# Performance work log

Measured on AMD Instinct MI355X. Metric: run time of the kernel, lower is better.

## Reference

```python
import jax, jax.numpy as jnp
import numpy as np

# config dims (see shape_source)
NO = 8        # Max_Object
NT = 32       # Max_Time
C = 512       # feat_dims
VD = 1024     # visual_dim
RD = 300      # self.nfeat (relation word-vector dim)
H = 4         # headnum
B = 8         # batch
No = NT * 2 * NO      # 512 object-graph nodes
Nr = NT * NO * NO     # 2048 relation-graph nodes


def _glorot(key, shape):
    fan_in = shape[0]
    return jax.random.normal(key, shape, dtype=jnp.float32) / np.sqrt(fan_in)


def setup_inputs() -> dict:
    key = jax.random.key(0)
    ks = jax.random.split(key, 18)
    inp = {
        "Ao": jax.random.uniform(ks[0], (B, No, No), dtype=jnp.float32),
        "srco": jax.random.normal(ks[1], (B, 1, 1, No, VD), dtype=jnp.float32),
        "Ar": jax.random.uniform(ks[2], (B, Nr, Nr), dtype=jnp.float32),
        "srcr": jax.random.normal(ks[3], (B, 1, 1, Nr, RD), dtype=jnp.float32),
        # GraphConvolution weights: gcl_o/gcl2_o and gcl_r/gcl2_r
        "Wo1": _glorot(ks[4], (VD, 1024)),
        "Wo2": _glorot(ks[5], (1024, C)),
        "Wr1": _glorot(ks[6], (RD, 1024)),
        "Wr2": _glorot(ks[7], (1024, C)),
        # MultiHeadAttention (e2n) projections
        "Wq": _glorot(ks[8], (C, C)), "bq": jnp.zeros((C,), jnp.float32),
        "Wk": _glorot(ks[9], (C, C)), "bk": jnp.zeros((C,), jnp.float32),
        "Wv": _glorot(ks[10], (C, C)), "bv": jnp.zeros((C,), jnp.float32),
        "Wp": _glorot(ks[11], (C, C)), "bp": jnp.zeros((C,), jnp.float32),
        # e2n_embed: Linear(2C -> C)
        "We": _glorot(ks[12], (2 * C, C)), "be": jnp.zeros((C,), jnp.float32),
    }
    return inp


def _gcn2(A, x, W1, W2):
    """Two stacked GraphConvolution layers with self-loops: relu((A+I) @ x @ W).
    A: (b,N,N), x: (b,N,Din). Vectorized over batch (torch code loops per-sample)."""
    eye = jnp.eye(A.shape[-1], dtype=A.dtype)
    Ah = A + eye
    h = jax.nn.relu(jnp.einsum('bij,bjd->bid', Ah, x @ W1))
    return jax.nn.relu(jnp.einsum('bij,bjd->bid', Ah, h @ W2))


def _mha(x, Wq, bq, Wk, bk, Wv, bv, Wp, bp):
    """Standard multi-head self-attention. x: (Bseg, S, C)."""
    Bs, S, _ = x.shape
    dh = C // H
    q = (x @ Wq + bq).reshape(Bs, S, H, dh)
    k = (x @ Wk + bk).reshape(Bs, S, H, dh)
    v = (x @ Wv + bv).reshape(Bs, S, H, dh)
    attn = jax.nn.softmax(jnp.einsum('bqhd,bkhd->bhqk', q, k) / np.sqrt(dh), axis=-1)
    o = jnp.einsum('bhqk,bkhd->bqhd', attn, v).reshape(Bs, S, C)
    return o @ Wp + bp


def _forward(Ao, srco, Ar, srcr, Wo1, Wo2, Wr1, Wr2,
             Wq, bq, Wk, bk, Wv, bv, Wp, bp, We, be):
    b = Ao.shape[0]
    # object-graph GCN (torch loops over batch; vectorized here)
    xo = srco[:, 0, 0, :, :VD]                       # (b, No, VD)
    srco_gcn = _gcn2(Ao, xo, Wo1, Wo2)               # (b, No, C)
    out_gcn_o = srco_gcn.reshape(b, NT, 2 * NO, C)
    # relation-graph GCN
    xr = srcr[:, 0, 0]                               # (b, Nr, RD)
    srcr_gcn = _gcn2(Ar, xr, Wr1, Wr2)               # (b, Nr, C)
    out_gcn_r = srcr_gcn.reshape(b, NT, NO * NO, C)
    # compute_e2n: segment-wise MHA over NO-token windows (torch loops over NO)
    r = out_gcn_r.reshape(b * NT, NO, NO, C)
    seg_a = r.reshape(b * NT * NO, NO, C)                      # rows of NOxNO grid
    a = _mha(seg_a, Wq, bq, Wk, bk, Wv, bv, Wp, bp).mean(axis=1)
    a = a.reshape(b * NT, NO, C)
    seg_o = jnp.swapaxes(r, 1, 2).reshape(b * NT * NO, NO, C)  # cols (permute 0,2,1,3)
    o = _mha(seg_o, Wq, bq, Wk, bk, Wv, bv, Wp, bp).mean(axis=1)
    o = o.reshape(b * NT, NO, C)
    tmp = jnp.concatenate([a, o], axis=1)                      # (b*NT, 2*NO, C)
    cat = jnp.concatenate([tmp, out_gcn_o.reshape(b * NT, 2 * NO, C)], axis=-1)
    out_e2n = cat @ We + be
    return out_e2n.reshape(b, NT, 2 * NO, C)


def reference(Ao, srco, Ar, srcr, Wo1, Wo2, Wr1, Wr2,
              Wq, bq, Wk, bk, Wv, bv, Wp, bp, We, be):
    return _forward(Ao, srco, Ar, srcr, Wo1, Wo2, Wr1, Wr2,
                    Wq, bq, Wk, bk, Wv, bv, Wp, bp, We, be)
```

## Files before the change

### kernel.cpp

```cpp
#include <hip/hip_runtime.h>
#include <hip/hip_bf16.h>


typedef __attribute__((ext_vector_type(4))) float f32x4;
typedef __attribute__((ext_vector_type(8))) short bf16x8s;

#define TILE 128
#define BKK 32
#define LDSS 40
#define LDSL 32

#if __has_builtin(__builtin_amdgcn_global_load_lds)
#define HAVE_GLL 1
#else
#define HAVE_GLL 0
#endif

__device__ inline void gll16(const __hip_bfloat16* g, __hip_bfloat16* l) {
#if HAVE_GLL
    __builtin_amdgcn_global_load_lds(
        (const __attribute__((address_space(1))) void*)g,
        (__attribute__((address_space(3))) void*)l,
        16, 0, 0);
#endif
}

__device__ inline void split2(float a, float b, unsigned& h, unsigned& l) {
    __hip_bfloat16 ha = __float2bfloat16(a), hb = __float2bfloat16(b);
    float ra = __bfloat162float(ha), rb = __bfloat162float(hb);
    __hip_bfloat16 la = __float2bfloat16(a - ra), lb = __float2bfloat16(b - rb);
    unsigned short uha = *(unsigned short*)&ha, uhb = *(unsigned short*)&hb;
    unsigned short ula = *(unsigned short*)&la, ulb = *(unsigned short*)&lb;
    h = (unsigned)uha | ((unsigned)uhb << 16);
    l = (unsigned)ula | ((unsigned)ulb << 16);
}

__device__ inline void splitw(float v, unsigned short& h, unsigned short& l) {
    __hip_bfloat16 hb = __float2bfloat16(v);
    __hip_bfloat16 lb = __float2bfloat16(v - __bfloat162float(hb));
    h = *(unsigned short*)&hb;
    l = *(unsigned short*)&lb;
}

__device__ inline void swz_block(int& bx, int& by, int& bz) {
    int gx = gridDim.x, gy = gridDim.y;
    int nwg = gx * gy * gridDim.z;
    int flat = bx + gx * (by + gy * bz);
    int cpx = nwg >> 3;
    int w = (flat & 7) * cpx + (flat >> 3);
    bx = w % gx;
    int t = w / gx;
    by = t % gy;
    bz = t / gy;
}

__global__ __launch_bounds__(256) void gemm_planes(
    const __hip_bfloat16* __restrict__ Aph, const __hip_bfloat16* __restrict__ Apl,
    long long sA, int lda,
    const __hip_bfloat16* __restrict__ BTh, const __hip_bfloat16* __restrict__ BTl,
    long long sBT, int ldbt,
    void* __restrict__ D, __hip_bfloat16* __restrict__ Dl_, long long sD, int ldd,
    const float* __restrict__ addN, long long sAddN, int ldaddN,
    const __hip_bfloat16* __restrict__ addTh, const __hip_bfloat16* __restrict__ addTl,
    long long sAddT, int ldaddT,
    const float* __restrict__ bias,
    int K, int relu, int outMode)
{
    __shared__ __hip_bfloat16 AhB[2][TILE * LDSL], AlB[2][TILE * LDSL];
    __shared__ __hip_bfloat16 BhB[2][TILE * LDSL], BlB[2][TILE * LDSL];

    int bx = blockIdx.x, by = blockIdx.y, bz = blockIdx.z;
    swz_block(bx, by, bz);

    const int tid  = threadIdx.x;
    const int lane = tid & 63;
    const int wave = tid >> 6;
    const int wm   = (wave >> 1) * 64;
    const int wn   = (wave & 1) * 64;
    const int row0 = by * TILE;
    const int col0 = bx * TILE;
    const int b    = bz;

    const __hip_bfloat16* Abh = Aph + (size_t)b * sA;
    const __hip_bfloat16* Abl = Apl + (size_t)b * sA;
    const __hip_bfloat16* Bbh = BTh + (size_t)b * sBT;
    const __hip_bfloat16* Bbl = BTl + (size_t)b * sBT;

    f32x4 acc[4][4];
#pragma unroll
    for (int i = 0; i < 4; ++i)
#pragma unroll
        for (int j = 0; j < 4; ++j) acc[i][j] = (f32x4){0.f, 0.f, 0.f, 0.f};

    const int quad = lane >> 4;
    const int l16  = lane & 15;

    const int m0  = wave * 16 + (lane >> 2);
    const int m1  = (wave + 4) * 16 + (lane >> 2);
    const int sl  = lane & 3;
    const int kq0 = sl ^ ((m0 >> 1) & 3);
    const int kq1 = sl ^ ((m1 >> 1) & 3);
    const size_t gA0 = (size_t)(row0 + m0) * lda + kq0 * 8;
    const size_t gA1 = (size_t)(row0 + m1) * lda + kq1 * 8;
    const size_t gB0 = (size_t)(col0 + m0) * ldbt + kq0 * 8;
    const size_t gB1 = (size_t)(col0 + m1) * ldbt + kq1 * 8;
    const int ldsc0 = wave * 512;
    const int ldsc1 = (wave + 4) * 512;

#if HAVE_GLL
#define STAGE(buf, kk) do { \
    gll16(Abh + gA0 + (kk), &AhB[buf][ldsc0]); \
    gll16(Abh + gA1 + (kk), &AhB[buf][ldsc1]); \
    gll16(Abl + gA0 + (kk), &AlB[buf][ldsc0]); \
    gll16(Abl + gA1 + (kk), &AlB[buf][ldsc1]); \
    gll16(Bbh + gB0 + (kk), &BhB[buf][ldsc0]); \
    gll16(Bbh + gB1 + (kk), &BhB[buf][ldsc1]); \
    gll16(Bbl + gB0 + (kk), &BlB[buf][ldsc0]); \
    gll16(Bbl + gB1 + (kk), &BlB[buf][ldsc1]); \
} while (0)
#else
#define STAGE(buf, kk) do { \
    *(uint4*)(&AhB[buf][m0 * LDSL + sl * 8]) = *(const uint4*)(Abh + gA0 + (kk)); \
    *(uint4*)(&AhB[buf][m1 * LDSL + sl * 8]) = *(const uint4*)(Abh + gA1 + (kk)); \
    *(uint4*)(&AlB[buf][m0 * LDSL + sl * 8]) = *(const uint4*)(Abl + gA0 + (kk)); \
    *(uint4*)(&AlB[buf][m1 * LDSL + sl * 8]) = *(const uint4*)(Abl + gA1 + (kk)); \
    *(uint4*)(&BhB[buf][m0 * LDSL + sl * 8]) = *(const uint4*)(Bbh + gB0 + (kk)); \
    *(uint4*)(&BhB[buf][m1 * LDSL + sl * 8]) = *(const uint4*)(Bbh + gB1 + (kk)); \
    *(uint4*)(&BlB[buf][m0 * LDSL + sl * 8]) = *(const uint4*)(Bbl + gB0 + (kk)); \
    *(uint4*)(&BlB[buf][m1 * LDSL + sl * 8]) = *(const uint4*)(Bbl + gB1 + (kk)); \
} while (0)
#endif

#if HAVE_GLL
#define WAITVM8() asm volatile("s_waitcnt vmcnt(8)" ::: "memory")
#define WAITVM0() asm volatile("s_waitcnt vmcnt(0)" ::: "memory")
#else
#define WAITVM8() asm volatile("" ::: "memory")
#define WAITVM0() asm volatile("" ::: "memory")
#endif

    const int nt = K / BKK;
    int cur = 0;

    STAGE(0, 0);
    STAGE(1, BKK);

    for (int t = 0; t < nt; ++t) {
        if (t + 1 < nt) { WAITVM8(); } else { WAITVM0(); }
        __builtin_amdgcn_s_barrier();

        const __hip_bfloat16* Ah = AhB[cur];
        const __hip_bfloat16* Al = AlB[cur];
        const __hip_bfloat16* Bh = BhB[cur];
        const __hip_bfloat16* Bl = BlB[cur];

        bf16x8s bhf[4], blf[4];
#pragma unroll
        for (int nt2 = 0; nt2 < 4; ++nt2) {
            int r = wn + nt2 * 16 + l16;
            int ss = (quad ^ ((r >> 1) & 3)) * 8;
            bhf[nt2] = *(const bf16x8s*)(&Bh[r * LDSL + ss]);
            blf[nt2] = *(const bf16x8s*)(&Bl[r * LDSL + ss]);
        }
#pragma unroll
        for (int mt = 0; mt < 4; ++mt) {
            int r = wm + mt * 16 + l16;
            int ss = (quad ^ ((r >> 1) & 3)) * 8;
            bf16x8s ahf = *(const bf16x8s*)(&Ah[r * LDSL + ss]);
            bf16x8s alf = *(const bf16x8s*)(&Al[r * LDSL + ss]);
#pragma unroll
            for (int nt2 = 0; nt2 < 4; ++nt2) {
                acc[mt][nt2] = __builtin_amdgcn_mfma_f32_16x16x32_bf16(ahf, bhf[nt2], acc[mt][nt2], 0, 0, 0);
                acc[mt][nt2] = __builtin_amdgcn_mfma_f32_16x16x32_bf16(ahf, blf[nt2], acc[mt][nt2], 0, 0, 0);
                acc[mt][nt2] = __builtin_amdgcn_mfma_f32_16x16x32_bf16(alf, bhf[nt2], acc[mt][nt2], 0, 0, 0);
            }
        }

        __builtin_amdgcn_s_barrier();
        if (t + 2 < nt) STAGE(cur, (t + 2) * BKK);
        cur ^= 1;
    }
#undef STAGE
#undef WAITVM8
#undef WAITVM0

    float* DbF = (float*)D + (size_t)b * sD;
    __hip_bfloat16* Dhb = (__hip_bfloat16*)D + (size_t)b * sD;
    __hip_bfloat16* Dlb = Dl_ ? Dl_ + (size_t)b * sD : nullptr;
    const float* AddN = addN ? addN + (size_t)b * sAddN : nullptr;
    const __hip_bfloat16* ATh = addTh ? addTh + (size_t)b * sAddT : nullptr;
    const __hip_bfloat16* ATl = addTl ? addTl + (size_t)b * sAddT : nullptr;
#pragma unroll
    for (int mt = 0; mt < 4; ++mt)
#pragma unroll
        for (int nt2 = 0; nt2 < 4; ++nt2)
#pragma unroll
            for (int r = 0; r < 4; ++r) {
                int m = row0 + wm + mt * 16 + quad * 4 + r;
                int n = col0 + wn + nt2 * 16 + l16;
                float v = acc[mt][nt2][r];
                if (AddN) v += AddN[(size_t)m * ldaddN + n];
                if (ATh) v += __bfloat162float(ATh[(size_t)n * ldaddT + m])
                            + __bfloat162float(ATl[(size_t)n * ldaddT + m]);
                if (bias) v += bias[n];
                if (relu && v < 0.f) v = 0.f;
                if (outMode == 0) {
                    DbF[(size_t)m * ldd + n] = v;
                } else {
                    unsigned short hh, ll;
                    splitw(v, hh, ll);
                    size_t o = (size_t)m * ldd + n;
                    *(unsigned short*)&Dhb[o] = hh;
                    *(unsigned short*)&Dlb[o] = ll;
                }
            }
}

__global__ __launch_bounds__(256) void gemm_asplit(
    const float* __restrict__ A, long long sA, int lda,
    const __hip_bfloat16* __restrict__ BTh, const __hip_bfloat16* __restrict__ BTl,
    long long sBT, int ldbt,
    __hip_bfloat16* __restrict__ Dh_, __hip_bfloat16* __restrict__ Dl_,
    long long sD, int ldd,
    const float* __restrict__ addN, long long sAddN, int ldaddN,
    const __hip_bfloat16* __restrict__ addTh, const __hip_bfloat16* __restrict__ addTl,
    long long sAddT, int ldaddT,
    int K, int relu)
{
    __shared__ __hip_bfloat16 Ah[TILE * LDSS], Al[TILE * LDSS];
    __shared__ __hip_bfloat16 Bh[TILE * LDSS], Bl[TILE * LDSS];

    const int tid  = threadIdx.x;
    const int lane = tid & 63;
    const int wave = tid >> 6;
    const int wm   = (wave >> 1) * 64;
    const int wn   = (wave & 1) * 64;
    const int row0 = blockIdx.y * TILE;
    const int col0 = blockIdx.x * TILE;
    const int b    = blockIdx.z;

    const float* Ab = A + (size_t)b * sA;
    const __hip_bfloat16* Bbh = BTh + (size_t)b * sBT;
    const __hip_bfloat16* Bbl = BTl + (size_t)b * sBT;

    f32x4 acc[4][4];
#pragma unroll
    for (int i = 0; i < 4; ++i)
#pragma unroll
        for (int j = 0; j < 4; ++j) acc[i][j] = (f32x4){0.f, 0.f, 0.f, 0.f};

    const int quad = lane >> 4;
    const int l16  = lane & 15;

    for (int k0 = 0; k0 < K; k0 += BKK) {
        __syncthreads();
#pragma unroll
        for (int it = 0; it < 2; ++it) {
            int task = tid + it * 256;
            int m = task >> 2, kq = task & 3;
            const float* ap = Ab + (size_t)(row0 + m) * lda + k0 + kq * 8;
            float4 v0 = *(const float4*)ap;
            float4 v1 = *(const float4*)(ap + 4);
            uint4 H, L;
            split2(v0.x, v0.y, H.x, L.x); split2(v0.z, v0.w, H.y, L.y);
            split2(v1.x, v1.y, H.z, L.z); split2(v1.z, v1.w, H.w, L.w);
            *(uint4*)(&Ah[m * LDSS + kq * 8]) = H;
            *(uint4*)(&Al[m * LDSS + kq * 8]) = L;
        }
#pragma unroll
        for (int it = 0; it < 2; ++it) {
            int task = tid + it * 256;
            int n = task >> 2, kq = task & 3;
            size_t off = (size_t)(col0 + n) * ldbt + k0 + kq * 8;
            *(uint4*)(&Bh[n * LDSS + kq * 8]) = *(const uint4*)(Bbh + off);
            *(uint4*)(&Bl[n * LDSS + kq * 8]) = *(const uint4*)(Bbl + off);
        }
        __syncthreads();

        bf16x8s ah[4], al[4], bh[4], bl[4];
#pragma unroll
        for (int mt = 0; mt < 4; ++mt) {
            int r = (wm + mt * 16 + l16) * LDSS + quad * 8;
            ah[mt] = *(const bf16x8s*)(&Ah[r]);
            al[mt] = *(const bf16x8s*)(&Al[r]);
        }
#pragma unroll
        for (int nt = 0; nt < 4; ++nt) {
            int r = (wn + nt * 16 + l16) * LDSS + quad * 8;
            bh[nt] = *(const bf16x8s*)(&Bh[r]);
            bl[nt] = *(const bf16x8s*)(&Bl[r]);
        }
#pragma unroll
        for (int mt = 0; mt < 4; ++mt)
#pragma unroll
            for (int nt = 0; nt < 4; ++nt) {
                acc[mt][nt] = __builtin_amdgcn_mfma_f32_16x16x32_bf16(ah[mt], bh[nt], acc[mt][nt], 0, 0, 0);
                acc[mt][nt] = __builtin_amdgcn_mfma_f32_16x16x32_bf16(ah[mt], bl[nt], acc[mt][nt], 0, 0, 0);
                acc[mt][nt] = __builtin_amdgcn_mfma_f32_16x16x32_bf16(al[mt], bh[nt], acc[mt][nt], 0, 0, 0);
            }
    }

    __hip_bfloat16* Dhb = Dh_ + (size_t)b * sD;
    __hip_bfloat16* Dlb = Dl_ + (size_t)b * sD;
    const float* AddN = addN ? addN + (size_t)b * sAddN : nullptr;
    const __hip_bfloat16* ATh = addTh ? addTh + (size_t)b * sAddT : nullptr;
    const __hip_bfloat16* ATl = addTl ? addTl + (size_t)b * sAddT : nullptr;
#pragma unroll
    for (int mt = 0; mt < 4; ++mt)
#pragma unroll
        for (int nt = 0; nt < 4; ++nt)
#pragma unroll
            for (int r = 0; r < 4; ++r) {
                int m = row0 + wm + mt * 16 + quad * 4 + r;
                int n = col0 + wn + nt * 16 + l16;
                float v = acc[mt][nt][r];
                if (AddN) v += AddN[(size_t)m * ldaddN + n];
                if (ATh) v += __bfloat162float(ATh[(size_t)n * ldaddT + m])
                            + __bfloat162float(ATl[(size_t)n * ldaddT + m]);
                if (relu && v < 0.f) v = 0.f;
                unsigned short hh, ll;
                splitw(v, hh, ll);
                size_t o = (size_t)m * ldd + n;
                *(unsigned short*)&Dhb[o] = hh;
                *(unsigned short*)&Dlb[o] = ll;
            }
}

__global__ __launch_bounds__(256) void padtrans_split(
    const float* __restrict__ src,
    __hip_bfloat16* __restrict__ dsth, __hip_bfloat16* __restrict__ dstl,
    int R, int C, int Rp, int Cp)
{
    __shared__ float T[64][65];
    const int t = threadIdx.x;
    const int tr = t >> 4, tc = t & 15;
    const int c0 = blockIdx.x * 64, r0 = blockIdx.y * 64;
    const size_t bat = blockIdx.z;
    const float* sb = src + bat * (size_t)R * C;
    __hip_bfloat16* dhb = dsth + bat * (size_t)Cp * Rp;
    __hip_bfloat16* dlb = dstl + bat * (size_t)Cp * Rp;

#pragma unroll
    for (int i = 0; i < 4; ++i) {
        int rr = tr + i * 16;
        int gr = r0 + rr;
        float v0 = 0.f, v1 = 0.f, v2 = 0.f, v3 = 0.f;
        if (gr < R) {
            int c = c0 + tc * 4;
            const float* s = sb + (size_t)gr * C + c;
            if (c + 0 < C) v0 = s[0];
            if (c + 1 < C) v1 = s[1];
            if (c + 2 < C) v2 = s[2];
            if (c + 3 < C) v3 = s[3];
        }
        T[rr][tc * 4 + 0] = v0; T[rr][tc * 4 + 1] = v1;
        T[rr][tc * 4 + 2] = v2; T[rr][tc * 4 + 3] = v3;
    }
    __syncthreads();
#pragma unroll
    for (int i = 0; i < 4; ++i) {
        int cc = tr + i * 16;
        float4 v = { T[tc * 4 + 0][cc], T[tc * 4 + 1][cc],
                     T[tc * 4 + 2][cc], T[tc * 4 + 3][cc] };
        ushort4 H, L;
        splitw(v.x, H.x, L.x); splitw(v.y, H.y, L.y);
        splitw(v.z, H.z, L.z); splitw(v.w, H.w, L.w);
        size_t off = (size_t)(c0 + cc) * Rp + r0 + tc * 4;
        *(ushort4*)(dhb + off) = H;
        *(ushort4*)(dlb + off) = L;
    }
}

__global__ __launch_bounds__(256) void gemm_bf16(
    const __hip_bfloat16* __restrict__ A, long long sA, int lda,
    const __hip_bfloat16* __restrict__ B, long long sB, int ldb,
    void* __restrict__ D, long long sD, int ldd,
    const __hip_bfloat16* __restrict__ addsrc, long long sAdd, int ldadd,
    const float* __restrict__ bias,
    int K, int relu, int outF32)
{
    __shared__ __hip_bfloat16 As[TILE * LDSS];
    __shared__ __hip_bfloat16 Bs[TILE * LDSS];

    int bx = blockIdx.x, by = blockIdx.y, bz = blockIdx.z;
    swz_block(bx, by, bz);

    const int tid  = threadIdx.x;
    const int lane = tid & 63;
    const int wave = tid >> 6;
    const int wm   = (wave >> 1) * 64;
    const int wn   = (wave & 1) * 64;
    const int row0 = by * TILE;
    const int col0 = bx * TILE;
    const int b    = bz;

    const __hip_bfloat16* Ab = A + (size_t)b * sA;
    const __hip_bfloat16* Bb = B + (size_t)b * sB;

    f32x4 acc[4][4];
#pragma unroll
    for (int i = 0; i < 4; ++i)
#pragma unroll
        for (int j = 0; j < 4; ++j) acc[i][j] = (f32x4){0.f, 0.f, 0.f, 0.f};

    const int quad = lane >> 4;
    const int l16  = lane & 15;

    for (int k0 = 0; k0 < K; k0 += BKK) {
        __syncthreads();
#pragma unroll
        for (int it = 0; it < 2; ++it) {
            int task = tid + it * 256;
            int m = task >> 2, kq = task & 3;
            uint4 val = *(const uint4*)(Ab + (size_t)(row0 + m) * lda + k0 + kq * 8);
            *(uint4*)(&As[m * LDSS + kq * 8]) = val;
        }
#pragma unroll
        for (int it = 0; it < 2; ++it) {
            int task = tid + it * 256;
            int kk = task >> 4, n8 = task & 15;
            uint4 val = *(const uint4*)(Bb + (size_t)(k0 + kk) * ldb + col0 + n8 * 8);
            const __hip_bfloat16* v16 = (const __hip_bfloat16*)&val;
#pragma unroll
            for (int u = 0; u < 8; ++u)
                Bs[(n8 * 8 + u) * LDSS + kk] = v16[u];
        }
        __syncthreads();

        bf16x8s afrag[4], bfrag[4];
#pragma unroll
        for (int mt = 0; mt < 4; ++mt)
            afrag[mt] = *(const bf16x8s*)(&As[(wm + mt * 16 + l16) * LDSS + quad * 8]);
#pragma unroll
        for (int nt = 0; nt < 4; ++nt)
            bfrag[nt] = *(const bf16x8s*)(&Bs[(wn + nt * 16 + l16) * LDSS + quad * 8]);
#pragma unroll
        for (int mt = 0; mt < 4; ++mt)
#pragma unroll
            for (int nt = 0; nt < 4; ++nt)
                acc[mt][nt] = __builtin_amdgcn_mfma_f32_16x16x32_bf16(
                    afrag[mt], bfrag[nt], acc[mt][nt], 0, 0, 0);
    }

    __hip_bfloat16* Db16 = (__hip_bfloat16*)D + (size_t)b * sD;
    float*          DbF  = (float*)D + (size_t)b * sD;
    const __hip_bfloat16* Addb = addsrc ? addsrc + (size_t)b * sAdd : nullptr;
#pragma unroll
    for (int mt = 0; mt < 4; ++mt)
#pragma unroll
        for (int nt = 0; nt < 4; ++nt)
#pragma unroll
            for (int r = 0; r < 4; ++r) {
                int m = row0 + wm + mt * 16 + quad * 4 + r;
                int n = col0 + wn + nt * 16 + l16;
                float v = acc[mt][nt][r];
                if (Addb) v += __bfloat162float(Addb[(size_t)m * ldadd + n]);
                if (bias) v += bias[n];
                if (relu && v < 0.f) v = 0.f;
                if (outF32) DbF[(size_t)m * ldd + n] = v;
                else        Db16[(size_t)m * ldd + n] = __float2bfloat16(v);
            }
}

__global__ void convert_kernel(const float* __restrict__ src,
                               __hip_bfloat16* __restrict__ dst, int n4)
{
    int i = blockIdx.x * blockDim.x + threadIdx.x;
    if (i >= n4) return;
    float4 v = ((const float4*)src)[i];
    __hip_bfloat16 t0 = __float2bfloat16(v.x), t1 = __float2bfloat16(v.y);
    __hip_bfloat16 t2 = __float2bfloat16(v.z), t3 = __float2bfloat16(v.w);
    ushort4 o = { *(unsigned short*)&t0, *(unsigned short*)&t1,
                  *(unsigned short*)&t2, *(unsigned short*)&t3 };
    ((ushort4*)dst)[i] = o;
}

__global__ void split_kernel(const float* __restrict__ src,
                             __hip_bfloat16* __restrict__ dh,
                             __hip_bfloat16* __restrict__ dl, int n4)
{
    int i = blockIdx.x * blockDim.x + threadIdx.x;
    if (i >= n4) return;
    float4 v = ((const float4*)src)[i];
    ushort4 H, L;
    splitw(v.x, H.x, L.x); splitw(v.y, H.y, L.y);
    splitw(v.z, H.z, L.z); splitw(v.w, H.w, L.w);
    ((ushort4*)dh)[i] = H;
    ((ushort4*)dl)[i] = L;
}

__global__ __launch_bounds__(256) void attn_kernel(
    const float* __restrict__ q,
    const float* __restrict__ k,
    const float* __restrict__ v,
    __hip_bfloat16* __restrict__ abar)
{
    __shared__ float qs[8][512], ks[8][512], vs[8][512];
    __shared__ float sc[4][8][8];
    __shared__ float wb[4][8];

    const int tid  = threadIdx.x;
    const int mode = blockIdx.y;
    const int g    = blockIdx.x >> 3;
    const int idx  = blockIdx.x & 7;
    const int rowBase = g * 64;

    for (int t = tid; t < 512; t += 256) {
        int p = t >> 6, c8 = (t & 63) * 8;
        int row = (mode == 0) ? (rowBase + idx * 8 + p) : (rowBase + p * 8 + idx);
        const float* qp = q + (size_t)row * 512 + c8;
        const float* kp = k + (size_t)row * 512 + c8;
        const float* vp = v + (size_t)row * 512 + c8;
        *(float4*)(&qs[p][c8])     = *(const float4*)(qp);
        *(float4*)(&qs[p][c8 + 4]) = *(const float4*)(qp + 4);
        *(float4*)(&ks[p][c8])     = *(const float4*)(kp);
        *(float4*)(&ks[p][c8 + 4]) = *(const float4*)(kp + 4);
        *(float4*)(&vs[p][c8])     = *(const float4*)(vp);
        *(float4*)(&vs[p][c8 + 4]) = *(const float4*)(vp + 4);
    }
    __syncthreads();

    {
        int h = tid >> 6, l = tid & 63;
        int i = l >> 3, j = l & 7;
        const float* qrow = &qs[i][h * 128];
        const float* krow = &ks[j][h * 128];
        float s = 0.f;
#pragma unroll
        for (int d = 0; d < 128; d += 4) {
            float4 qa = *(const float4*)(qrow + d);
            float4 kb = *(const float4*)(krow + d);
            s += qa.x * kb.x + qa.y * kb.y + qa.z * kb.z + qa.w * kb.w;
        }
        sc[h][i][j] = s * 0.08838834764831845f;
    }
    __syncthreads();

    if (tid < 32) {
        int h = tid >> 3, i = tid & 7;
        float mx = -1e30f;
#pragma unroll
        for (int j = 0; j < 8; ++j) mx = fmaxf(mx, sc[h][i][j]);
        float e[8], sum = 0.f;
#pragma unroll
        for (int j = 0; j < 8; ++j) { e[j] = __expf(sc[h][i][j] - mx); sum += e[j]; }
        float inv = 1.f / sum;
#pragma unroll
        for (int j = 0; j < 8; ++j) sc[h][i][j] = e[j] * inv;
    }
    __syncthreads();

    if (tid < 32) {
        int h = tid >> 3, j = tid & 7;
        float s = 0.f;
#pragma unroll
        for (int i = 0; i < 8; ++i) s += sc[h][i][j];
        wb[h][j] = s * 0.125f;
    }
    __syncthreads();

    {
        int orow = g * 16 + mode * 8 + idx;
        for (int c = tid; c < 512; c += 256) {
            int h = c >> 7;
            float o = 0.f;
#pragma unroll
            for (int j = 0; j < 8; ++j) o += wb[h][j] * vs[j][c];
            abar[(size_t)orow * 512 + c] = __float2bfloat16(o);
        }
    }
}


extern "C" void kernel_launch(void* const* d_in, const int* in_sizes, int n_in,
                              void* d_out, int out_size, void* d_ws, size_t ws_size,
                              hipStream_t stream)
{
    const float* Ao   = (const float*)d_in[0];
    const float* srco = (const float*)d_in[1];
    const float* Ar   = (const float*)d_in[2];
    const float* srcr = (const float*)d_in[3];
    const float* Wo1  = (const float*)d_in[4];
    const float* Wo2  = (const float*)d_in[5];
    const float* Wr1  = (const float*)d_in[6];
    const float* Wr2  = (const float*)d_in[7];
    const float* Wq   = (const float*)d_in[8];
    const float* bq   = (const float*)d_in[9];
    const float* Wk   = (const float*)d_in[10];
    const float* bk   = (const float*)d_in[11];
    const float* Wv   = (const float*)d_in[12];
    const float* bv   = (const float*)d_in[13];
    const float* Wp   = (const float*)d_in[14];
    const float* bp   = (const float*)d_in[15];
    const float* We   = (const float*)d_in[16];
    const float* be   = (const float*)d_in[17];
    float* out = (float*)d_out;

    char* ws = (char*)d_ws;
    const size_t R0 = 0;
    const size_t R1 = 67108864;
    const size_t R2 = 100663296;
    const size_t R3 = 134217728;
    const size_t R4 = 167772160;
    const size_t R5 = 192937984;
    const size_t R6 = 199491584;

    __hip_bfloat16* HRh = (__hip_bfloat16*)(ws + R0);
    __hip_bfloat16* HRl = HRh + 16777216;
    float* qF   = (float*)(ws + R0);
    float* kF   = (float*)(ws + R0 + 33554432);
    float* T2Rf = (float*)(ws + R1);
    float* vF   = (float*)(ws + R1);
    __hip_bfloat16* Uh = (__hip_bfloat16*)(ws + R2);
    __hip_bfloat16* Ul = Uh + 6291456;
    __hip_bfloat16* T2RTh = (__hip_bfloat16*)(ws + R2);
    __hip_bfloat16* T2RTl = T2RTh + 8388608;
    __hip_bfloat16* GRh = (__hip_bfloat16*)(ws + R3);
    __hip_bfloat16* GRl = GRh + 8388608;
    __hip_bfloat16* XPTh = (__hip_bfloat16*)(ws + R4);
    __hip_bfloat16* XPTl = XPTh + 6291456;
    __hip_bfloat16* ABAR = (__hip_bfloat16*)(ws + R4);
    __hip_bfloat16* WPTh = (__hip_bfloat16*)(ws + R5);
    __hip_bfloat16* WPTl = WPTh + 327680;
    __hip_bfloat16* Wr2Th = (__hip_bfloat16*)(ws + R5 + 1310720);
    __hip_bfloat16* Wr2Tl = Wr2Th + 524288;
    __hip_bfloat16* WqTh = (__hip_bfloat16*)(ws + R5 + 3407872);
    __hip_bfloat16* WqTl = WqTh + 262144;
    __hip_bfloat16* WkTh = (__hip_bfloat16*)(ws + R5 + 4456448);
    __hip_bfloat16* WkTl = WkTh + 262144;
    __hip_bfloat16* WvTh = (__hip_bfloat16*)(ws + R5 + 5505024);
    __hip_bfloat16* WvTl = WvTh + 262144;
    __hip_bfloat16* Arh = (__hip_bfloat16*)(ws + R6);
    __hip_bfloat16* Arl = Arh + 33554432;
    const bool haveArPlanes = ws_size >= R6 + 2ull * 67108864ull;

    __hip_bfloat16* TO    = (__hip_bfloat16*)(ws + R2 + 0);
    __hip_bfloat16* HO    = (__hip_bfloat16*)(ws + R2 + 8388608);
    __hip_bfloat16* T2O   = (__hip_bfloat16*)(ws + R2 + 16777216);
    __hip_bfloat16* CAT   = (__hip_bfloat16*)(ws + R2 + 20971520);
    __hip_bfloat16* srcoB = (__hip_bfloat16*)(ws + R2 + 29360128);
    __hip_bfloat16* AoB   = (__hip_bfloat16*)(ws + R2 + 37748736);
    __hip_bfloat16* Wo1B  = (__hip_bfloat16*)(ws + R2 + 41943040);
    __hip_bfloat16* Wo2B  = (__hip_bfloat16*)(ws + R2 + 44040192);
    __hip_bfloat16* WeB   = (__hip_bfloat16*)(ws + R2 + 45088768);
    __hip_bfloat16* WpB   = (__hip_bfloat16*)(ws + R2 + 46137344);

    dim3 blk(256);
    auto cvt = [&](const float* s, __hip_bfloat16* d, int n) {
        convert_kernel<<<dim3((n / 4 + 255) / 256), blk, 0, stream>>>(s, d, n / 4);
    };

    padtrans_split<<<dim3(6, 32, 8), blk, 0, stream>>>(srcr, XPTh, XPTl, 2048, 300, 2048, 384);
    padtrans_split<<<dim3(16, 5, 1), blk, 0, stream>>>(Wr1, WPTh, WPTl, 300, 1024, 320, 1024);
    padtrans_split<<<dim3(8, 16, 1), blk, 0, stream>>>(Wr2, Wr2Th, Wr2Tl, 1024, 512, 1024, 512);
    padtrans_split<<<dim3(8, 8, 1), blk, 0, stream>>>(Wq, WqTh, WqTl, 512, 512, 512, 512);
    padtrans_split<<<dim3(8, 8, 1), blk, 0, stream>>>(Wk, WkTh, WkTl, 512, 512, 512, 512);
    padtrans_split<<<dim3(8, 8, 1), blk, 0, stream>>>(Wv, WvTh, WvTl, 512, 512, 512, 512);

    if (haveArPlanes) {
        split_kernel<<<dim3(32768), blk, 0, stream>>>(Ar, Arh, Arl, 8388608);
        gemm_planes<<<dim3(3, 16, 8), blk, 0, stream>>>(
            Arh, Arl, 2048LL * 2048, 2048, XPTh, XPTl, 384LL * 2048, 2048,
            Uh, Ul, 2048LL * 384, 384,
            nullptr, 0, 0, XPTh, XPTl, 384LL * 2048, 2048,
            nullptr, 2048, 0, 1);
    } else {
        gemm_asplit<<<dim3(3, 16, 8), blk, 0, stream>>>(
            Ar, 2048LL * 2048, 2048, XPTh, XPTl, 384LL * 2048, 2048,
            Uh, Ul, 2048LL * 384, 384,
            nullptr, 0, 0, XPTh, XPTl, 384LL * 2048, 2048,
            2048, 0);
    }
    gemm_planes<<<dim3(8, 128, 1), blk, 0, stream>>>(
        Uh, Ul, 0, 384, WPTh, WPTl, 0, 320,
        HRh, HRl, 0, 1024,
        nullptr, 0, 0, nullptr, nullptr, 0, 0,
        nullptr, 320, 1, 1);
    gemm_planes<<<dim3(4, 128, 1), blk, 0, stream>>>(
        HRh, HRl, 0, 1024, Wr2Th, Wr2Tl, 0, 1024,
        T2Rf, nullptr, 0, 512,
        nullptr, 0, 0, nullptr, nullptr, 0, 0,
        nullptr, 1024, 0, 0);
    padtrans_split<<<dim3(8, 32, 8), blk, 0, stream>>>(T2Rf, T2RTh, T2RTl, 2048, 512, 2048, 512);
    if (haveArPlanes) {
        gemm_planes<<<dim3(4, 16, 8), blk, 0, stream>>>(
            Arh, Arl, 2048LL * 2048, 2048, T2RTh, T2RTl, 512LL * 2048, 2048,
            GRh, GRl, 2048LL * 512, 512,
            T2Rf, 2048LL * 512, 512, nullptr, nullptr, 0, 0,
            nullptr, 2048, 1, 1);
    } else {
        gemm_asplit<<<dim3(4, 16, 8), blk, 0, stream>>>(
            Ar, 2048LL * 2048, 2048, T2RTh, T2RTl, 512LL * 2048, 2048,
            GRh, GRl, 2048LL * 512, 512,
            T2Rf, 2048LL * 512, 512, nullptr, nullptr, 0, 0,
            2048, 1);
    }
    gemm_planes<<<dim3(4, 128, 1), blk, 0, stream>>>(
        GRh, GRl, 0, 512, WqTh, WqTl, 0, 512,
        qF, nullptr, 0, 512,
        nullptr, 0, 0, nullptr, nullptr, 0, 0,
        bq, 512, 0, 0);
    gemm_planes<<<dim3(4, 128, 1), blk, 0, stream>>>(
        GRh, GRl, 0, 512, WkTh, WkTl, 0, 512,
        kF, nullptr, 0, 512,
        nullptr, 0, 0, nullptr, nullptr, 0, 0,
        bk, 512, 0, 0);
    gemm_planes<<<dim3(4, 128, 1), blk, 0, stream>>>(
        GRh, GRl, 0, 512, WvTh, WvTl, 0, 512,
        vF, nullptr, 0, 512,
        nullptr, 0, 0, nullptr, nullptr, 0, 0,
        bv, 512, 0, 0);
    attn_kernel<<<dim3(2048, 2), blk, 0, stream>>>(qF, kF, vF, ABAR);

    cvt(srco, srcoB, 4194304);
    cvt(Ao, AoB, 2097152);
    cvt(Wo1, Wo1B, 1048576);
    cvt(Wo2, Wo2B, 524288);
    cvt(We, WeB, 524288);
    cvt(Wp, WpB, 262144);
    gemm_bf16<<<dim3(8, 32, 1), blk, 0, stream>>>(srcoB, 0, 1024, Wo1B, 0, 1024,
        TO, 0, 1024, nullptr, 0, 0, nullptr, 1024, 0, 0);
    gemm_bf16<<<dim3(8, 4, 8), blk, 0, stream>>>(AoB, 512LL * 512, 512, TO, 512LL * 1024, 1024,
        HO, 512LL * 1024, 1024, TO, 512LL * 1024, 1024, nullptr, 512, 1, 0);
    gemm_bf16<<<dim3(4, 32, 1), blk, 0, stream>>>(HO, 0, 1024, Wo2B, 0, 512,
        T2O, 0, 512, nullptr, 0, 0, nullptr, 1024, 0, 0);
    gemm_bf16<<<dim3(4, 4, 8), blk, 0, stream>>>(AoB, 512LL * 512, 512, T2O, 512LL * 512, 512,
        (void*)(CAT + 512), 512LL * 1024, 1024, T2O, 512LL * 512, 512, nullptr, 512, 1, 0);
    gemm_bf16<<<dim3(4, 32, 1), blk, 0, stream>>>(ABAR, 0, 512, WpB, 0, 512,
        CAT, 0, 1024, nullptr, 0, 0, bp, 512, 0, 0);
    gemm_bf16<<<dim3(4, 32, 1), blk, 0, stream>>>(CAT, 0, 1024, WeB, 0, 512,
        out, 0, 512, nullptr, 0, 0, be, 1024, 0, 1);
}
```

Baseline: 1.132 ms.

## Fuse Q/K/V projections into one GEMM and add pipelined transposed-B bf16 GEMM

Concatenates the Wq/Wk/Wv weights and biases so the three projection GEMMs run as one wider launch writing an interleaved QKV buffer, and the attention kernel reads it with a stride. Adds a double-buffered, global-to-LDS pipelined bf16 GEMM that takes pre-transposed bf16 weights, and uses it for the four dense weight GEMMs on the object and e2n path. The aim is to cut launch count, reuse the A tiles across Q/K/V, and speed up the plain bf16 GEMMs. The cost is a few extra transpose and bias-concat kernels plus a wider strided QKV layout.

```diff
diff --git a/kernel.cpp b/kernel.cpp
--- a/kernel.cpp
+++ b/kernel.cpp
@@ -118,6 +118,8 @@
     gll16(Bbl + gB0 + (kk), &BlB[buf][ldsc0]); \
     gll16(Bbl + gB1 + (kk), &BlB[buf][ldsc1]); \
 } while (0)
+#define WAITVM8() asm volatile("s_waitcnt vmcnt(8)" ::: "memory")
+#define WAITVM0() asm volatile("s_waitcnt vmcnt(0)" ::: "memory")
 #else
 #define STAGE(buf, kk) do { \
     *(uint4*)(&AhB[buf][m0 * LDSL + sl * 8]) = *(const uint4*)(Abh + gA0 + (kk)); \
@@ -129,12 +131,6 @@
     *(uint4*)(&BlB[buf][m0 * LDSL + sl * 8]) = *(const uint4*)(Bbl + gB0 + (kk)); \
     *(uint4*)(&BlB[buf][m1 * LDSL + sl * 8]) = *(const uint4*)(Bbl + gB1 + (kk)); \
 } while (0)
-#endif
-
-#if HAVE_GLL
-#define WAITVM8() asm volatile("s_waitcnt vmcnt(8)" ::: "memory")
-#define WAITVM0() asm volatile("s_waitcnt vmcnt(0)" ::: "memory")
-#else
 #define WAITVM8() asm volatile("" ::: "memory")
 #define WAITVM0() asm volatile("" ::: "memory")
 #endif
@@ -216,6 +212,124 @@
             }
 }
 
+__global__ __launch_bounds__(256) void gemm_bf16t(
+    const __hip_bfloat16* __restrict__ A, int lda,
+    const __hip_bfloat16* __restrict__ BT, int ldbt,
+    void* __restrict__ D, int ldd,
+    const float* __restrict__ bias,
+    int K, int outF32)
+{
+    __shared__ __hip_bfloat16 AsB[2][TILE * LDSL];
+    __shared__ __hip_bfloat16 BsB[2][TILE * LDSL];
+
+    int bx = blockIdx.x, by = blockIdx.y, bz = blockIdx.z;
+    swz_block(bx, by, bz);
+
+    const int tid  = threadIdx.x;
+    const int lane = tid & 63;
+    const int wave = tid >> 6;
+    const int wm   = (wave >> 1) * 64;
+    const int wn   = (wave & 1) * 64;
+    const int row0 = by * TILE;
+    const int col0 = bx * TILE;
+
+    f32x4 acc[4][4];
+#pragma unroll
+    for (int i = 0; i < 4; ++i)
+#pragma unroll
+        for (int j = 0; j < 4; ++j) acc[i][j] = (f32x4){0.f, 0.f, 0.f, 0.f};
+
+    const int quad = lane >> 4;
+    const int l16  = lane & 15;
+
+    const int m0  = wave * 16 + (lane >> 2);
+    const int m1  = (wave + 4) * 16 + (lane >> 2);
+    const int sl  = lane & 3;
+    const int kq0 = sl ^ ((m0 >> 1) & 3);
+    const int kq1 = sl ^ ((m1 >> 1) & 3);
+    const size_t gA0 = (size_t)(row0 + m0) * lda + kq0 * 8;
+    const size_t gA1 = (size_t)(row0 + m1) * lda + kq1 * 8;
+    const size_t gB0 = (size_t)(col0 + m0) * ldbt + kq0 * 8;
+    const size_t gB1 = (size_t)(col0 + m1) * ldbt + kq1 * 8;
+    const int ldsc0 = wave * 512;
+    const int ldsc1 = (wave + 4) * 512;
+
+#if HAVE_GLL
+#define STAGE1(buf, kk) do { \
+    gll16(A + gA0 + (kk), &AsB[buf][ldsc0]); \
+    gll16(A + gA1 + (kk), &AsB[buf][ldsc1]); \
+    gll16(BT + gB0 + (kk), &BsB[buf][ldsc0]); \
+    gll16(BT + gB1 + (kk), &BsB[buf][ldsc1]); \
+} while (0)
+#define WAITVM4() asm volatile("s_waitcnt vmcnt(4)" ::: "memory")
+#define WAITVM0() asm volatile("s_waitcnt vmcnt(0)" ::: "memory")
+#else
+#define STAGE1(buf, kk) do { \
+    *(uint4*)(&AsB[buf][m0 * LDSL + sl * 8]) = *(const uint4*)(A + gA0 + (kk)); \
+    *(uint4*)(&AsB[buf][m1 * LDSL + sl * 8]) = *(const uint4*)(A + gA1 + (kk)); \
+    *(uint4*)(&BsB[buf][m0 * LDSL + sl * 8]) = *(const uint4*)(BT + gB0 + (kk)); \
+    *(uint4*)(&BsB[buf][m1 * LDSL + sl * 8]) = *(const uint4*)(BT + gB1 + (kk)); \
+} while (0)
+#define WAITVM4() asm volatile("" ::: "memory")
+#define WAITVM0() asm volatile("" ::: "memory")
+#endif
+
+    const int nt = K / BKK;
+    int cur = 0;
+
+    STAGE1(0, 0);
+    STAGE1(1, BKK);
+
+    for (int t = 0; t < nt; ++t) {
+        if (t + 1 < nt) { WAITVM4(); } else { WAITVM0(); }
+        __builtin_amdgcn_s_barrier();
+
+        const __hip_bfloat16* As = AsB[cur];
+        const __hip_bfloat16* Bs = BsB[cur];
+
+        bf16x8s bfrag[4];
+#pragma unroll
+        for (int nt2 = 0; nt2 < 4; ++nt2) {
+            int r = wn + nt2 * 16 + l16;
+            int ss = (quad ^ ((r >> 1) & 3)) * 8;
+            bfrag[nt2] = *(const bf16x8s*)(&Bs[r * LDSL + ss]);
+        }
+#pragma unroll
+        for (int mt = 0; mt < 4; ++mt) {
+            int r = wm + mt * 16 + l16;
+            int ss = (quad ^ ((r >> 1) & 3)) * 8;
+            bf16x8s afrag = *(const bf16x8s*)(&As[r * LDSL + ss]);
+#pragma unroll
+            for (int nt2 = 0; nt2 < 4; ++nt2)
+                acc[mt][nt2] = __builtin_amdgcn_mfma_f32_16x16x32_bf16(
+                    afrag, bfrag[nt2], acc[mt][nt2], 0, 0, 0);
+        }
+
+        __builtin_amdgcn_s_barrier();
+        if (t + 2 < nt) STAGE1(cur, (t + 2) * BKK);
+        cur ^= 1;
+    }
+#undef STAGE1
+#undef WAITVM4
+#undef WAITVM0
+
+    float* DbF = (float*)D;
+    __hip_bfloat16* Db16 = (__hip_bfloat16*)D;
+#pragma unroll
+    for (int mt = 0; mt < 4; ++mt)
+#pragma unroll
+        for (int nt2 = 0; nt2 < 4; ++nt2)
+#pragma unroll
+            for (int r = 0; r < 4; ++r) {
+                int m = row0 + wm + mt * 16 + quad * 4 + r;
+                int n = col0 + wn + nt2 * 16 + l16;
+                float v = acc[mt][nt2][r];
+                if (bias) v += bias[n];
+                if (outF32) DbF[(size_t)m * ldd + n] = v;
+                else        Db16[(size_t)m * ldd + n] = __float2bfloat16(v);
+            }
+}
+
 __global__ __launch_bounds__(256) void gemm_asplit(
     const float* __restrict__ A, long long sA, int lda,
     const __hip_bfloat16* __restrict__ BTh, const __hip_bfloat16* __restrict__ BTl,
@@ -371,6 +485,45 @@
     }
 }
 
+__global__ __launch_bounds__(256) void padtrans_bf16(
+    const float* __restrict__ src, __hip_bfloat16* __restrict__ dst,
+    int R, int C, int Rp, int Cp)
+{
+    __shared__ float T[64][65];
+    const int t = threadIdx.x;
+    const int tr = t >> 4, tc = t & 15;
+    const int c0 = blockIdx.x * 64, r0 = blockIdx.y * 64;
+
+#pragma unroll
+    for (int i = 0; i < 4; ++i) {
+        int rr = tr + i * 16;
+        int gr = r0 + rr;
+        float v0 = 0.f, v1 = 0.f, v2 = 0.f, v3 = 0.f;
+        if (gr < R) {
+            int c = c0 + tc * 4;
+            const float* s = src + (size_t)gr * C + c;
+            if (c + 0 < C) v0 = s[0];
+            if (c + 1 < C) v1 = s[1];
+            if (c + 2 < C) v2 = s[2];
+            if (c + 3 < C) v3 = s[3];
+        }
+        T[rr][tc * 4 + 0] = v0; T[rr][tc * 4 + 1] = v1;
+        T[rr][tc * 4 + 2] = v2; T[rr][tc * 4 + 3] = v3;
+    }
+    __syncthreads();
+#pragma unroll
+    for (int i = 0; i < 4; ++i) {
+        int cc = tr + i * 16;
+        __hip_bfloat16 b0 = __float2bfloat16(T[tc * 4 + 0][cc]);
+        __hip_bfloat16 b1 = __float2bfloat16(T[tc * 4 + 1][cc]);
+        __hip_bfloat16 b2 = __float2bfloat16(T[tc * 4 + 2][cc]);
+        __hip_bfloat16 b3 = __float2bfloat16(T[tc * 4 + 3][cc]);
+        ushort4 o = { *(unsigned short*)&b0, *(unsigned short*)&b1,
+                      *(unsigned short*)&b2, *(unsigned short*)&b3 };
+        *(ushort4*)(dst + (size_t)(c0 + cc) * Rp + r0 + tc * 4) = o;
+    }
+}
+
 __global__ __launch_bounds__(256) void gemm_bf16(
     const __hip_bfloat16* __restrict__ A, long long sA, int lda,
     const __hip_bfloat16* __restrict__ B, long long sB, int ldb,
@@ -489,10 +642,22 @@
     ((ushort4*)dl)[i] = L;
 }
 
+__global__ void bcat_kernel(const float* __restrict__ b0,
+                            const float* __restrict__ b1,
+                            const float* __restrict__ b2,
+                            float* __restrict__ dst)
+{
+    int i = blockIdx.x * blockDim.x + threadIdx.x;
+    if (i >= 1536) return;
+    float v = (i < 512) ? b0[i] : (i < 1024) ? b1[i - 512] : b2[i - 1024];
+    dst[i] = v;
+}
+
 __global__ __launch_bounds__(256) void attn_kernel(
     const float* __restrict__ q,
     const float* __restrict__ k,
     const float* __restrict__ v,
+    int ld,
     __hip_bfloat16* __restrict__ abar)
 {
     __shared__ float qs[8][512], ks[8][512], vs[8][512];
@@ -508,9 +673,9 @@
     for (int t = tid; t < 512; t += 256) {
         int p = t >> 6, c8 = (t & 63) * 8;
         int row = (mode == 0) ? (rowBase + idx * 8 + p) : (rowBase + p * 8 + idx);
-        const float* qp = q + (size_t)row * 512 + c8;
-        const float* kp = k + (size_t)row * 512 + c8;
-        const float* vp = v + (size_t)row * 512 + c8;
+        const float* qp = q + (size_t)row * ld + c8;
+        const float* kp = k + (size_t)row * ld + c8;
+        const float* vp = v + (size_t)row * ld + c8;
         *(float4*)(&qs[p][c8])     = *(const float4*)(qp);
         *(float4*)(&qs[p][c8 + 4]) = *(const float4*)(qp + 4);
         *(float4*)(&ks[p][c8])     = *(const float4*)(kp);
@@ -607,14 +772,13 @@
 
     __hip_bfloat16* HRh = (__hip_bfloat16*)(ws + R0);
     __hip_bfloat16* HRl = HRh + 16777216;
-    float* qF   = (float*)(ws + R0);
-    float* kF   = (float*)(ws + R0 + 33554432);
+    float* QKV  = (float*)(ws + R0);
     float* T2Rf = (float*)(ws + R1);
-    float* vF   = (float*)(ws + R1);
     __hip_bfloat16* Uh = (__hip_bfloat16*)(ws + R2);
     __hip_bfloat16* Ul = Uh + 6291456;
     __hip_bfloat16* T2RTh = (__hip_bfloat16*)(ws + R2);
     __hip_bfloat16* T2RTl = T2RTh + 8388608;
+    float* bqkv = (float*)(ws + R2);
     __hip_bfloat16* GRh = (__hip_bfloat16*)(ws + R3);
     __hip_bfloat16* GRl = GRh + 8388608;
     __hip_bfloat16* XPTh = (__hip_bfloat16*)(ws + R4);
@@ -624,26 +788,22 @@
     __hip_bfloat16* WPTl = WPTh + 327680;
     __hip_bfloat16* Wr2Th = (__hip_bfloat16*)(ws + R5 + 1310720);
     __hip_bfloat16* Wr2Tl = Wr2Th + 524288;
-    __hip_bfloat16* WqTh = (__hip_bfloat16*)(ws + R5 + 3407872);
-    __hip_bfloat16* WqTl = WqTh + 262144;
-    __hip_bfloat16* WkTh = (__hip_bfloat16*)(ws + R5 + 4456448);
-    __hip_bfloat16* WkTl = WkTh + 262144;
-    __hip_bfloat16* WvTh = (__hip_bfloat16*)(ws + R5 + 5505024);
-    __hip_bfloat16* WvTl = WvTh + 262144;
+    __hip_bfloat16* WqkvTh = (__hip_bfloat16*)(ws + R5 + 3407872);
+    __hip_bfloat16* WqkvTl = (__hip_bfloat16*)(ws + R5 + 4980736);
     __hip_bfloat16* Arh = (__hip_bfloat16*)(ws + R6);
     __hip_bfloat16* Arl = Arh + 33554432;
     const bool haveArPlanes = ws_size >= R6 + 2ull * 67108864ull;
 
-    __hip_bfloat16* TO    = (__hip_bfloat16*)(ws + R2 + 0);
-    __hip_bfloat16* HO    = (__hip_bfloat16*)(ws + R2 + 8388608);
-    __hip_bfloat16* T2O   = (__hip_bfloat16*)(ws + R2 + 16777216);
-    __hip_bfloat16* CAT   = (__hip_bfloat16*)(ws + R2 + 20971520);
-    __hip_bfloat16* srcoB = (__hip_bfloat16*)(ws + R2 + 29360128);
-    __hip_bfloat16* AoB   = (__hip_bfloat16*)(ws + R2 + 37748736);
-    __hip_bfloat16* Wo1B  = (__hip_bfloat16*)(ws + R2 + 41943040);
-    __hip_bfloat16* Wo2B  = (__hip_bfloat16*)(ws + R2 + 44040192);
-    __hip_bfloat16* WeB   = (__hip_bfloat16*)(ws + R2 + 45088768);
-    __hip_bfloat16* WpB   = (__hip_bfloat16*)(ws + R2 + 46137344);
+    __hip_bfloat16* TO     = (__hip_bfloat16*)(ws + R2 + 0);
+    __hip_bfloat16* HO     = (__hip_bfloat16*)(ws + R2 + 8388608);
+    __hip_bfloat16* T2O    = (__hip_bfloat16*)(ws + R2 + 16777216);
+    __hip_bfloat16* CAT    = (__hip_bfloat16*)(ws + R2 + 20971520);
+    __hip_bfloat16* srcoB  = (__hip_bfloat16*)(ws + R2 + 29360128);
+    __hip_bfloat16* AoB    = (__hip_bfloat16*)(ws + R2 + 37748736);
+    __hip_bfloat16* Wo1BT  = (__hip_bfloat16*)(ws + R2 + 41943040);
+    __hip_bfloat16* Wo2BT  = (__hip_bfloat16*)(ws + R2 + 44040192);
+    __hip_bfloat16* WeBT   = (__hip_bfloat16*)(ws + R2 + 45088768);
+    __hip_bfloat16* WpBT   = (__hip_bfloat16*)(ws + R2 + 46137344);
 
     dim3 blk(256);
     auto cvt = [&](const float* s, __hip_bfloat16* d, int n) {
@@ -653,9 +813,9 @@
     padtrans_split<<<dim3(6, 32, 8), blk, 0, stream>>>(srcr, XPTh, XPTl, 2048, 300, 2048, 384);
     padtrans_split<<<dim3(16, 5, 1), blk, 0, stream>>>(Wr1, WPTh, WPTl, 300, 1024, 320, 1024);
     padtrans_split<<<dim3(8, 16, 1), blk, 0, stream>>>(Wr2, Wr2Th, Wr2Tl, 1024, 512, 1024, 512);
-    padtrans_split<<<dim3(8, 8, 1), blk, 0, stream>>>(Wq, WqTh, WqTl, 512, 512, 512, 512);
-    padtrans_split<<<dim3(8, 8, 1), blk, 0, stream>>>(Wk, WkTh, WkTl, 512, 512, 512, 512);
-    padtrans_split<<<dim3(8, 8, 1), blk, 0, stream>>>(Wv, WvTh, WvTl, 512, 512, 512, 512);
+    padtrans_split<<<dim3(8, 8, 1), blk, 0, stream>>>(Wq, WqkvTh, WqkvTl, 512, 512, 512, 512);
+    padtrans_split<<<dim3(8, 8, 1), blk, 0, stream>>>(Wk, WqkvTh + 262144, WqkvTl + 262144, 512, 512, 512, 512);
+    padtrans_split<<<dim3(8, 8, 1), blk, 0, stream>>>(Wv, WqkvTh + 524288, WqkvTl + 524288, 512, 512, 512, 512);
 
     if (haveArPlanes) {
         split_kernel<<<dim3(32768), blk, 0, stream>>>(Ar, Arh, Arl, 8388608);
@@ -695,39 +855,30 @@
             T2Rf, 2048LL * 512, 512, nullptr, nullptr, 0, 0,
             2048, 1);
     }
-    gemm_planes<<<dim3(4, 128, 1), blk, 0, stream>>>(
-        GRh, GRl, 0, 512, WqTh, WqTl, 0, 512,
-        qF, nullptr, 0, 512,
+    bcat_kernel<<<dim3(6), blk, 0, stream>>>(bq, bk, bv, bqkv);
+    gemm_planes<<<dim3(12, 128, 1), blk, 0, stream>>>(
+        GRh, GRl, 0, 512, WqkvTh, WqkvTl, 0, 512,
+        QKV, nullptr, 0, 1536,
         nullptr, 0, 0, nullptr, nullptr, 0, 0,
-        bq, 512, 0, 0);
-    gemm_planes<<<dim3(4, 128, 1), blk, 0, stream>>>(
-        GRh, GRl, 0, 512, WkTh, WkTl, 0, 512,
-        kF, nullptr, 0, 512,
-        nullptr, 0, 0, nullptr, nullptr, 0, 0,
-        bk, 512, 0, 0);
-    gemm_planes<<<dim3(4, 128, 1), blk, 0, stream>>>(
-        GRh, GRl, 0, 512, WvTh, WvTl, 0, 512,
-        vF, nullptr, 0, 512,
-        nullptr, 0, 0, nullptr, nullptr, 0, 0,
-        bv, 512, 0, 0);
-    attn_kernel<<<dim3(2048, 2), blk, 0, stream>>>(qF, kF, vF, ABAR);
+        bqkv, 512, 0, 0);
+    attn_kernel<<<dim3(2048, 2), blk, 0, stream>>>(QKV, QKV + 512, QKV + 1024, 1536, ABAR);
 
     cvt(srco, srcoB, 4194304);
     cvt(Ao, AoB, 2097152);
-    cvt(Wo1, Wo1B, 1048576);
-    cvt(Wo2, Wo2B, 524288);
-    cvt(We, WeB, 524288);
-    cvt(Wp, WpB, 262144);
-    gemm_bf16<<<dim3(8, 32, 1), blk, 0, stream>>>(srcoB, 0, 1024, Wo1B, 0, 1024,
-        TO, 0, 1024, nullptr, 0, 0, nullptr, 1024, 0, 0);
+    padtrans_bf16<<<dim3(16, 16, 1), blk, 0, stream>>>(Wo1, Wo1BT, 1024, 1024, 1024, 1024);
+    padtrans_bf16<<<dim3(8, 16, 1), blk, 0, stream>>>(Wo2, Wo2BT, 1024, 512, 1024, 512);
+    padtrans_bf16<<<dim3(8, 16, 1), blk, 0, stream>>>(We, WeBT, 1024, 512, 1024, 512);
+    padtrans_bf16<<<dim3(8, 8, 1), blk, 0, stream>>>(Wp, WpBT, 512, 512, 512, 512);
+    gemm_bf16t<<<dim3(8, 32, 1), blk, 0, stream>>>(srcoB, 1024, Wo1BT, 1024,
+        TO, 1024, nullptr, 1024, 0);
     gemm_bf16<<<dim3(8, 4, 8), blk, 0, stream>>>(AoB, 512LL * 512, 512, TO, 512LL * 1024, 1024,
         HO, 512LL * 1024, 1024, TO, 512LL * 1024, 1024, nullptr, 512, 1, 0);
-    gemm_bf16<<<dim3(4, 32, 1), blk, 0, stream>>>(HO, 0, 1024, Wo2B, 0, 512,
-        T2O, 0, 512, nullptr, 0, 0, nullptr, 1024, 0, 0);
+    gemm_bf16t<<<dim3(4, 32, 1), blk, 0, stream>>>(HO, 1024, Wo2BT, 1024,
+        T2O, 512, nullptr, 1024, 0);
     gemm_bf16<<<dim3(4, 4, 8), blk, 0, stream>>>(AoB, 512LL * 512, 512, T2O, 512LL * 512, 512,
         (void*)(CAT + 512), 512LL * 1024, 1024, T2O, 512LL * 512, 512, nullptr, 512, 1, 0);
-    gemm_bf16<<<dim3(4, 32, 1), blk, 0, stream>>>(ABAR, 0, 512, WpB, 0, 512,
-        CAT, 0, 1024, nullptr, 0, 0, bp, 512, 0, 0);
-    gemm_bf16<<<dim3(4, 32, 1), blk, 0, stream>>>(CAT, 0, 1024, WeB, 0, 512,
-        out, 0, 512, nullptr, 0, 0, be, 1024, 0, 1);
-}
+    gemm_bf16t<<<dim3(4, 32, 1), blk, 0, stream>>>(ABAR, 512, WpBT, 512,
+        CAT, 1024, bp, 512, 0);
+    gemm_bf16t<<<dim3(4, 32, 1), blk, 0, stream>>>(CAT, 1024, WeBT, 1024,
+        out, 512, be, 1024, 1);
+}
```

Result: faster. 1.015 ms (-10.4%).
